# Performance work log

Measured on AMD Instinct MI355X. Metric: run time of the kernel, lower is better.

## Reference

```python
import jax, jax.numpy as jnp
import numpy as np

B, C, H, W = 8, 64, 64, 64
HID = 256  # hidden width of gate_strength_fc


def _init_params(key):
    ks = jax.random.split(key, 12)
    s = 0.05
    p = {}
    p['Wq'] = jax.random.normal(ks[0], (C, C), jnp.float32) * s
    p['bq'] = jnp.zeros((C,), jnp.float32)
    p['Wk'] = jax.random.normal(ks[1], (C, C), jnp.float32) * s
    p['bk'] = jnp.zeros((C,), jnp.float32)
    p['Wv'] = jax.random.normal(ks[2], (C, C), jnp.float32) * s
    p['bv'] = jnp.zeros((C,), jnp.float32)
    p['Wg'] = jax.random.normal(ks[3], (C, C), jnp.float32) * s
    p['bg'] = jnp.zeros((C,), jnp.float32)
    p['W1'] = jax.random.normal(ks[4], (HID, C), jnp.float32) * s
    p['b1'] = jnp.zeros((HID,), jnp.float32)
    p['W2'] = jax.random.normal(ks[5], (1, HID), jnp.float32) * s
    p['b2'] = jnp.zeros((1,), jnp.float32)
    return p


def setup_inputs() -> dict:
    key = jax.random.key(0)
    k0, k1, k2, kp = jax.random.split(key, 4)
    x = jax.random.normal(k0, (B, C, H, W), jnp.float32)
    # torch.rand(...) > 0.8 dropout-style mask, precomputed as 0/1 float for determinism
    mask = (jax.random.uniform(k1, (B, 1, H, W), jnp.float32) > 0.8).astype(jnp.float32)
    use_entropy_gate = jax.random.bernoulli(k2, 0.5, (B,))
    inp = {'x': x, 'mask': mask, 'use_entropy_gate': use_entropy_gate}
    inp.update(_init_params(kp))
    return inp


def _conv1x1(w, b, t):
    # 1x1 conv == per-pixel matmul over channels
    return jnp.einsum('oc,bchw->bohw', w, t) + b[None, :, None, None]


def reference(x, mask, use_entropy_gate, Wq, bq, Wk, bk, Wv, bv, Wg, bg, W1, b1, W2, b2):
    b_, c_, h_, w_ = x.shape
    n = h_ * w_
    masked_x = x * mask
    q = _conv1x1(Wq, bq, masked_x).reshape(b_, c_, n).transpose(0, 2, 1)  # [B,N,C]
    k = _conv1x1(Wk, bk, masked_x).reshape(b_, c_, n)                      # [B,C,N]
    v = _conv1x1(Wv, bv, x).reshape(b_, c_, n)                             # [B,C,N]
    attn = jax.nn.softmax(jnp.einsum('bnc,bcm->bnm', q, k), axis=-1)       # [B,N,N]
    out = jnp.einsum('bcn,bmn->bcm', v, attn).reshape(b_, c_, h_, w_)
    hidden = jax.nn.relu(_conv1x1(W1, b1, x))
    gate_strength = jax.nn.sigmoid(_conv1x1(W2, b2, hidden))               # [B,1,H,W]
    gate = jax.nn.sigmoid(_conv1x1(Wg, bg, x))                             # [B,C,H,W]
    flag = use_entropy_gate[:, None, None, None]
    return jnp.where(flag, out * gate * gate_strength, x)
```

## Files before the change

### kernel.cpp

```cpp
#include <hip/hip_runtime.h>
#include <hip/hip_bf16.h>
#include <math.h>

namespace {
constexpr int kB = 8;
constexpr int kC = 64;
constexpr int kN = 4096;
constexpr int kCap = 1280;
constexpr int kQS = 1312;
constexpr int kSplit = 2;
constexpr long kSeg = (long)kB * kC * kN;
typedef __attribute__((ext_vector_type(8))) short short8;
typedef __attribute__((ext_vector_type(4))) float f32x4;
}

__global__ __launch_bounds__(256) void dense_kernel(
    const float* __restrict__ x, const float* __restrict__ mask,
    const int* __restrict__ flag,
    const float* __restrict__ Wq, const float* __restrict__ bq,
    const float* __restrict__ Wk, const float* __restrict__ bk,
    const float* __restrict__ Wv, const float* __restrict__ bv,
    const float* __restrict__ Wg, const float* __restrict__ bg,
    const float* __restrict__ W1, const float* __restrict__ b1,
    const float* __restrict__ W2, const float* __restrict__ b2,
    __hip_bfloat16* __restrict__ G, float* __restrict__ GS,
    __hip_bfloat16* __restrict__ Qa, __hip_bfloat16* __restrict__ Ka,
    __hip_bfloat16* __restrict__ VaT, float* __restrict__ Sq,
    float* __restrict__ xmsP, int* __restrict__ p2i, int* __restrict__ cnt) {
  const int b = blockIdx.y;
  if (!flag[b]) return;
  const int tile = blockIdx.x;
  const int n0 = tile * 64;
  const int t = threadIdx.x;
  const int wid = t >> 6;
  const int lane = t & 63;

  __shared__ __hip_bfloat16 sWf[4096 * 8];
  __shared__ __hip_bfloat16 sX[64][72];
  __shared__ float sB[512];
  __shared__ float sW2[256];
  __shared__ int sRed[4];
  __shared__ int sI[64];

  {
    const int c = t >> 2;
    const int nn = (t & 3) * 16;
    const float* xp = x + (long)b * kC * kN + (long)c * kN + n0 + nn;
#pragma unroll
    for (int u = 0; u < 16; ++u) sX[nn + u][c] = __float2bfloat16(xp[u]);
  }
  if (t < 64) { sB[t] = bq[t]; sB[64 + t] = bk[t]; sB[128 + t] = bv[t]; sB[192 + t] = bg[t]; }
  sB[256 + t] = b1[t];
  sW2[t] = W2[t];
  for (int f = t; f < 4096; f += 256) {
    const int mt = f >> 7;
    const int ks = (f >> 6) & 1;
    const int ln = f & 63;
    const int m = mt * 16 + (ln & 15);
    const int k0 = ks * 32 + (ln >> 4) * 8;
    const float* Wsrc;
    int row;
    if (m < 64)       { Wsrc = Wq; row = m; }
    else if (m < 128) { Wsrc = Wk; row = m - 64; }
    else if (m < 192) { Wsrc = Wv; row = m - 128; }
    else if (m < 256) { Wsrc = Wg; row = m - 192; }
    else              { Wsrc = W1; row = m - 256; }
#pragma unroll
    for (int j = 0; j < 8; ++j)
      sWf[f * 8 + j] = __float2bfloat16(Wsrc[row * kC + k0 + j]);
  }
  int loc = 0;
  for (int n = t; n < n0; n += 256) loc += (mask[b * kN + n] != 0.f) ? 1 : 0;
#pragma unroll
  for (int d = 1; d < 64; d <<= 1) loc += __shfl_xor(loc, d);
  if (lane == 0) sRed[wid] = loc;
  __syncthreads();
  const int pbase = sRed[0] + sRed[1] + sRed[2] + sRed[3];
  if (wid == 0) {
    const bool a = mask[b * kN + n0 + lane] != 0.f;
    const unsigned long long bal = __ballot(a);
    int ia = a ? (pbase + (int)__popcll(bal & ((1ULL << lane) - 1ULL))) : -1;
    if (ia >= kCap) ia = -1;
    sI[lane] = ia;
    p2i[b * kN + n0 + lane] = ia;
    if (tile == 63 && lane == 0) cnt[b] = pbase + (int)__popcll(bal);
  }
  __syncthreads();

  const int col = lane & 15;
  const int quad = lane >> 4;
  const int nl = wid * 16 + col;
  const int n = n0 + nl;
  const short8 bfr0 = *(const short8*)&sX[nl][quad * 8];
  const short8 bfr1 = *(const short8*)&sX[nl][32 + quad * 8];
  const int i_act = sI[nl];
  const float b2v = b2[0];

  float gs_acc = 0.f;
  float sq_acc = 0.f;
  for (int mt = 0; mt < 32; ++mt) {
    const short8 a0 = *(const short8*)&sWf[((mt * 2 + 0) * 64 + lane) * 8];
    const short8 a1 = *(const short8*)&sWf[((mt * 2 + 1) * 64 + lane) * 8];
    f32x4 acc = {0.f, 0.f, 0.f, 0.f};
    acc = __builtin_amdgcn_mfma_f32_16x16x32_bf16(a0, bfr0, acc, 0, 0, 0);
    acc = __builtin_amdgcn_mfma_f32_16x16x32_bf16(a1, bfr1, acc, 0, 0, 0);
    const int rbase = mt * 16 + quad * 4;
    if (mt < 4) {
      if (i_act >= 0) {
#pragma unroll
        for (int g = 0; g < 4; ++g) {
          const int r = rbase + g;
          const float qv = acc[g] + sB[r];
          Qa[((long)b * kCap + i_act) * kC + r] = __float2bfloat16(qv);
          sq_acc += qv * sB[64 + r];
        }
      }
    } else if (mt < 8) {
      if (i_act >= 0) {
#pragma unroll
        for (int g = 0; g < 4; ++g) {
          const int r = rbase + g;
          Ka[((long)b * kCap + i_act) * kC + (r - 64)] = __float2bfloat16(acc[g] + sB[r]);
        }
      }
    } else if (mt < 12) {
      if (i_act >= 0) {
#pragma unroll
        for (int g = 0; g < 4; ++g) {
          const int r = rbase + g;
          VaT[((long)b * kC + (r - 128)) * kCap + i_act] =
              __float2bfloat16(acc[g] + sB[r]);
        }
      }
    } else if (mt < 16) {
#pragma unroll
      for (int g = 0; g < 4; ++g) {
        const int r = rbase + g;
        const float gv = 1.f / (1.f + __expf(-(acc[g] + sB[r])));
        G[((long)b * kC + (r - 192)) * kN + n] = __float2bfloat16(gv);
      }
    } else {
#pragma unroll
      for (int g = 0; g < 4; ++g) {
        const int r = rbase + g;
        gs_acc += sW2[r - 256] * fmaxf(acc[g] + sB[r], 0.f);
      }
    }
  }
  gs_acc += __shfl_xor(gs_acc, 16);
  gs_acc += __shfl_xor(gs_acc, 32);
  sq_acc += __shfl_xor(sq_acc, 16);
  sq_acc += __shfl_xor(sq_acc, 32);
  if (quad == 0) {
    GS[(long)b * kN + n] = 1.f / (1.f + __expf(-(gs_acc + b2v)));
    if (i_act >= 0) Sq[(long)b * kCap + i_act] = sq_acc;
  }
  {
    const int c = t >> 2;
    const int g4 = t & 3;
    const float* mp = mask + (long)b * kN + n0 + g4 * 16;
    float s = 0.f;
#pragma unroll
    for (int u = 0; u < 16; ++u)
      if (mp[u] == 0.f) s += __bfloat162float(sX[g4 * 16 + u][c]);
    s += __shfl_xor(s, 1);
    s += __shfl_xor(s, 2);
    if (g4 == 0) xmsP[((long)b * 64 + tile) * kC + c] = s;
  }
}

__global__ __launch_bounds__(64) void attn_act_kernel(
    const __hip_bfloat16* __restrict__ Qa, const __hip_bfloat16* __restrict__ Ka,
    const __hip_bfloat16* __restrict__ VaT,
    const int* __restrict__ cnt, const int* __restrict__ flag,
    const float* __restrict__ bq, const float* __restrict__ bk,
    const float* __restrict__ bv, const float* __restrict__ Wv,
    const float* __restrict__ xmsP,
    float* __restrict__ Pm, float* __restrict__ Pl,
    __hip_bfloat16* __restrict__ Po,
    float* __restrict__ Vsum, float* __restrict__ s0M) {
  const int b = blockIdx.z;
  if (!flag[b]) return;
  const int lane = threadIdx.x;

  __shared__ __hip_bfloat16 sP[16][40];
  __shared__ float sxm[kC];

  if (blockIdx.x == kQS / 16) {
    if (blockIdx.y != 0) return;
    float acc = 0.f;
    for (int k = 0; k < 64; ++k) acc += xmsP[((long)b * 64 + k) * kC + lane];
    sxm[lane] = acc;
    __syncthreads();
    float v = 0.f;
#pragma unroll
    for (int o = 0; o < kC; ++o) v += Wv[lane * kC + o] * sxm[o];
    Vsum[b * kC + lane] = v + (float)(kN - cnt[b]) * bv[lane];
    float pp = bq[lane] * bk[lane];
#pragma unroll
    for (int d = 1; d < 64; d <<= 1) pp += __shfl_xor(pp, d);
    if (lane == 0) s0M[0] = pp;
    return;
  }

  const int cc = min(cnt[b], kCap);
  const int ccq = cc + 1;
  const int q0 = blockIdx.x * 16;
  if (q0 >= ccq) return;
  const int s = blockIdx.y;
  const int col = lane & 15;
  const int quad = lane >> 4;
  const int gq = q0 + col;

  const int nT = (cc + 31) >> 5;
  const int tq = (nT + kSplit - 1) / kSplit;
  const int t0 = s * tq;
  const int t1 = min(t0 + tq, nT);
  const long pb = ((long)b * kSplit + s) * kQS + gq;

  if (t0 >= t1) {
    if (gq < ccq) {
      if (quad == 0) { Pm[pb] = -3e38f; Pl[pb] = 0.f; }
#pragma unroll
      for (int ct = 0; ct < 4; ++ct)
#pragma unroll
        for (int g = 0; g < 4; ++g)
          Po[pb * kC + ct * 16 + quad * 4 + g] = __float2bfloat16(0.f);
    }
    return;
  }

  short8 qf0, qf1;
  if (gq == cc) {
#pragma unroll
    for (int j = 0; j < 8; ++j) {
      ((__hip_bfloat16*)&qf0)[j] = __float2bfloat16(bq[quad * 8 + j]);
      ((__hip_bfloat16*)&qf1)[j] = __float2bfloat16(bq[32 + quad * 8 + j]);
    }
  } else {
    const int qrow = (gq < cc) ? gq : (cc - 1);
    const __hip_bfloat16* qr = Qa + ((long)b * kCap + qrow) * kC + quad * 8;
    qf0 = *(const short8*)(qr);
    qf1 = *(const short8*)(qr + 32);
  }

  float Mi = -3e38f, Li = 0.f;
  f32x4 oacc[4];
#pragma unroll
  for (int ct = 0; ct < 4; ++ct) oacc[ct] = (f32x4){0.f, 0.f, 0.f, 0.f};

  for (int kt = t0; kt < t1; ++kt) {
    const int i0 = kt * 32;
    const int kr0 = min(i0 + col, cc - 1);
    const int kr1 = min(i0 + 16 + col, cc - 1);
    const __hip_bfloat16* kp0 = Ka + ((long)b * kCap + kr0) * kC + quad * 8;
    const __hip_bfloat16* kp1 = Ka + ((long)b * kCap + kr1) * kC + quad * 8;
    const short8 kf00 = *(const short8*)(kp0);
    const short8 kf01 = *(const short8*)(kp0 + 32);
    const short8 kf10 = *(const short8*)(kp1);
    const short8 kf11 = *(const short8*)(kp1 + 32);

    f32x4 sa0 = {0.f, 0.f, 0.f, 0.f}, sa1 = {0.f, 0.f, 0.f, 0.f};
    sa0 = __builtin_amdgcn_mfma_f32_16x16x32_bf16(kf00, qf0, sa0, 0, 0, 0);
    sa0 = __builtin_amdgcn_mfma_f32_16x16x32_bf16(kf01, qf1, sa0, 0, 0, 0);
    sa1 = __builtin_amdgcn_mfma_f32_16x16x32_bf16(kf10, qf0, sa1, 0, 0, 0);
    sa1 = __builtin_amdgcn_mfma_f32_16x16x32_bf16(kf11, qf1, sa1, 0, 0, 0);

    float sc[8];
#pragma unroll
    for (int g = 0; g < 4; ++g) {
      sc[g]     = (i0 + quad * 4 + g < cc)      ? sa0[g] : -3e38f;
      sc[4 + g] = (i0 + 16 + quad * 4 + g < cc) ? sa1[g] : -3e38f;
    }
    float lm = sc[0];
#pragma unroll
    for (int u = 1; u < 8; ++u) lm = fmaxf(lm, sc[u]);
    lm = fmaxf(lm, __shfl_xor(lm, 16));
    lm = fmaxf(lm, __shfl_xor(lm, 32));
    const float newM = fmaxf(Mi, lm);
    const float alpha = __expf(Mi - newM);
    float p[8], ps = 0.f;
#pragma unroll
    for (int u = 0; u < 8; ++u) { p[u] = __expf(sc[u] - newM); ps += p[u]; }
    ps += __shfl_xor(ps, 16);
    ps += __shfl_xor(ps, 32);
    Li = Li * alpha + ps;
    Mi = newM;

#pragma unroll
    for (int g = 0; g < 4; ++g) {
      sP[col][quad * 4 + g] = __float2bfloat16(p[g]);
      sP[col][16 + quad * 4 + g] = __float2bfloat16(p[4 + g]);
    }
    __syncthreads();
    const short8 pf = *(const short8*)&sP[col][quad * 8];

#pragma unroll
    for (int ct = 0; ct < 4; ++ct)
#pragma unroll
      for (int g = 0; g < 4; ++g) oacc[ct][g] *= alpha;
#pragma unroll
    for (int ct = 0; ct < 4; ++ct) {
      const short8 vf = *(const short8*)(
          VaT + ((long)b * kC + ct * 16 + col) * kCap + i0 + quad * 8);
      oacc[ct] = __builtin_amdgcn_mfma_f32_16x16x32_bf16(vf, pf, oacc[ct], 0, 0, 0);
    }
    __syncthreads();
  }

  if (gq < ccq) {
    if (quad == 0) { Pm[pb] = Mi; Pl[pb] = Li; }
#pragma unroll
    for (int ct = 0; ct < 4; ++ct)
#pragma unroll
      for (int g = 0; g < 4; ++g)
        Po[pb * kC + ct * 16 + quad * 4 + g] = __float2bfloat16(oacc[ct][g]);
  }
}

__global__ __launch_bounds__(256) void epilogue_kernel(
    const float* __restrict__ x, const int* __restrict__ flag,
    const int* __restrict__ p2i, const int* __restrict__ cnt,
    const float* __restrict__ Pm, const float* __restrict__ Pl,
    const __hip_bfloat16* __restrict__ Po, const float* __restrict__ Sq,
    const float* __restrict__ s0M, const float* __restrict__ Vsum,
    const __hip_bfloat16* __restrict__ G, const float* __restrict__ GS,
    float* __restrict__ out) {
  const int b = blockIdx.z;
  const int cg = blockIdx.y;
  const int n = blockIdx.x * 256 + threadIdx.x;
  const int t = threadIdx.x;
  const long bbase = (long)b * kC * kN + n;
  if (!flag[b]) {
#pragma unroll
    for (int u = 0; u < 16; ++u) {
      const long a = bbase + (long)(cg * 16 + u) * kN;
      out[a] = x[a];
    }
    return;
  }
  const int cTrue = cnt[b];
  const int cc = min(cTrue, kCap);
  const float multF = (float)(kN - cTrue);

  __shared__ float sFac[kSplit + 1];
  __shared__ float sOM16[16];
  __shared__ float sVs[16];
  if (t == 0) {
    const float s0 = s0M[0];
    float mar[kSplit], lar[kSplit];
    float M = s0;
#pragma unroll
    for (int s = 0; s < kSplit; ++s) {
      const long pbs = ((long)b * kSplit + s) * kQS + cc;
      mar[s] = Pm[pbs];
      lar[s] = Pl[pbs];
      M = fmaxf(M, mar[s]);
    }
    const float p0 = __expf(s0 - M);
    float L = multF * p0;
    float wgt[kSplit];
#pragma unroll
    for (int s = 0; s < kSplit; ++s) { wgt[s] = __expf(mar[s] - M); L += lar[s] * wgt[s]; }
    const float invL = 1.f / L;
#pragma unroll
    for (int s = 0; s < kSplit; ++s) sFac[s] = wgt[s] * invL;
    sFac[kSplit] = p0 * invL;
  }
  if (t < 16) sVs[t] = Vsum[b * kC + cg * 16 + t];
  __syncthreads();
  if (t < 16) {
    const int c = cg * 16 + t;
    float o = sFac[kSplit] * sVs[t];
#pragma unroll
    for (int s = 0; s < kSplit; ++s)
      o += sFac[s] * __bfloat162float(Po[(((long)b * kSplit + s) * kQS + cc) * kC + c]);
    sOM16[t] = o;
  }
  __syncthreads();

  const float gsv = GS[(long)b * kN + n];
  const int i = p2i[b * kN + n];
  float r16[16];
  if (i >= 0) {
    const float s0 = Sq[(long)b * kCap + i];
    float mar[kSplit], lar[kSplit];
    float M = s0;
#pragma unroll
    for (int s = 0; s < kSplit; ++s) {
      const long pbs = ((long)b * kSplit + s) * kQS + i;
      mar[s] = Pm[pbs];
      lar[s] = Pl[pbs];
      M = fmaxf(M, mar[s]);
    }
    const float p0 = __expf(s0 - M);
    float L = multF * p0;
    float fac[kSplit];
#pragma unroll
    for (int s = 0; s < kSplit; ++s) { fac[s] = __expf(mar[s] - M); L += lar[s] * fac[s]; }
    const float invL = 1.f / L;
    const float facP = p0 * invL;
#pragma unroll
    for (int u = 0; u < 16; ++u) r16[u] = facP * sVs[u];
#pragma unroll
    for (int s = 0; s < kSplit; ++s) {
      const float f = fac[s] * invL;
      const __hip_bfloat16* pr =
          Po + (((long)b * kSplit + s) * kQS + i) * kC + cg * 16;
      const short8 po0 = *(const short8*)(pr);
      const short8 po1 = *(const short8*)(pr + 8);
#pragma unroll
      for (int u = 0; u < 8; ++u) {
        r16[u]     += f * __bfloat162float(((const __hip_bfloat16*)&po0)[u]);
        r16[8 + u] += f * __bfloat162float(((const __hip_bfloat16*)&po1)[u]);
      }
    }
  } else {
#pragma unroll
    for (int u = 0; u < 16; ++u) r16[u] = sOM16[u];
  }
#pragma unroll
  for (int u = 0; u < 16; ++u) {
    const long a = bbase + (long)(cg * 16 + u) * kN;
    out[a] = r16[u] * __bfloat162float(G[a]) * gsv;
  }
}

extern "C" void kernel_launch(void* const* d_in, const int* in_sizes, int n_in,
                              void* d_out, int out_size, void* d_ws, size_t ws_size,
                              hipStream_t stream) {
  (void)in_sizes; (void)n_in; (void)out_size; (void)ws_size;
  const float* x    = (const float*)d_in[0];
  const float* mask = (const float*)d_in[1];
  const int*   flag = (const int*)d_in[2];
  const float* Wq = (const float*)d_in[3];
  const float* bq = (const float*)d_in[4];
  const float* Wk = (const float*)d_in[5];
  const float* bk = (const float*)d_in[6];
  const float* Wv = (const float*)d_in[7];
  const float* bv = (const float*)d_in[8];
  const float* Wg = (const float*)d_in[9];
  const float* bg = (const float*)d_in[10];
  const float* W1 = (const float*)d_in[11];
  const float* b1 = (const float*)d_in[12];
  const float* W2 = (const float*)d_in[13];
  const float* b2 = (const float*)d_in[14];
  float* out = (float*)d_out;

  char* w = (char*)d_ws;
  float* GS = (float*)w;                       w += (long)kB * kN * 4;
  __hip_bfloat16* G  = (__hip_bfloat16*)w;     w += kSeg * 2;
  __hip_bfloat16* Qa = (__hip_bfloat16*)w;     w += (long)kB * kCap * kC * 2;
  __hip_bfloat16* Ka = (__hip_bfloat16*)w;     w += (long)kB * kCap * kC * 2;
  __hip_bfloat16* VaT= (__hip_bfloat16*)w;     w += (long)kB * kC * kCap * 2;
  __hip_bfloat16* Po = (__hip_bfloat16*)w;     w += (long)kB * kSplit * kQS * kC * 2;
  float* Pm = (float*)w;                       w += (long)kB * kSplit * kQS * 4;
  float* Pl = (float*)w;                       w += (long)kB * kSplit * kQS * 4;
  float* Sq = (float*)w;                       w += (long)kB * kCap * 4;
  float* xmsP = (float*)w;                     w += (long)kB * 64 * kC * 4;
  int* p2i = (int*)w;                          w += (long)kB * kN * 4;
  int* cnt = (int*)w;                          w += 64;
  float* Vsum = (float*)w;                     w += kB * kC * 4;
  float* s0M  = (float*)w;                     w += 64;

  dim3 gd(64, kB);
  dense_kernel<<<gd, 256, 0, stream>>>(x, mask, flag, Wq, bq, Wk, bk, Wv, bv,
                                       Wg, bg, W1, b1, W2, b2,
                                       G, GS, Qa, Ka, VaT, Sq, xmsP, p2i, cnt);
  dim3 gat(kQS / 16 + 1, kSplit, kB);
  attn_act_kernel<<<gat, 64, 0, stream>>>(Qa, Ka, VaT, cnt, flag, bq, bk, bv, Wv,
                                          xmsP, Pm, Pl, Po, Vsum, s0M);
  dim3 gep(kN / 256, 4, kB);
  epilogue_kernel<<<gep, 256, 0, stream>>>(x, flag, p2i, cnt, Pm, Pl, Po, Sq,
                                           s0M, Vsum, G, GS, out);
}
```

Baseline: 122.4 us.

## Split attention key tiles across 8 waves per block with in-LDS merge

Replaces the 2-way split-K across separate 64-thread blocks with 512-thread blocks whose 8 waves each process interleaved key tiles. The waves merge their online-softmax partials (max, sum, output) through shared memory, so the epilogue reads one partial instead of combining several. K fragments for the next tile are prefetched and V loads are issued early. The __syncthreads in the loop become a wave-local LDS wait. The aim is more parallelism per query tile and less partial-result traffic. In exchange, each block uses more LDS and pays a cross-wave reduction step.

```diff
diff --git a/kernel.cpp b/kernel.cpp
--- a/kernel.cpp
+++ b/kernel.cpp
@@ -8,7 +8,7 @@
 constexpr int kN = 4096;
 constexpr int kCap = 1280;
 constexpr int kQS = 1312;
-constexpr int kSplit = 2;
+constexpr int kW = 8;
 constexpr long kSeg = (long)kB * kC * kN;
 typedef __attribute__((ext_vector_type(8))) short short8;
 typedef __attribute__((ext_vector_type(4))) float f32x4;
@@ -169,7 +169,7 @@
   }
 }
 
-__global__ __launch_bounds__(64) void attn_act_kernel(
+__global__ __launch_bounds__(512) void attn_act_kernel(
     const __hip_bfloat16* __restrict__ Qa, const __hip_bfloat16* __restrict__ Ka,
     const __hip_bfloat16* __restrict__ VaT,
     const int* __restrict__ cnt, const int* __restrict__ flag,
@@ -179,22 +179,19 @@
     float* __restrict__ Pm, float* __restrict__ Pl,
     __hip_bfloat16* __restrict__ Po,
     float* __restrict__ Vsum, float* __restrict__ s0M) {
-  const int b = blockIdx.z;
+  const int b = blockIdx.y;
   if (!flag[b]) return;
-  const int lane = threadIdx.x;
-
-  __shared__ __hip_bfloat16 sP[16][40];
-  __shared__ float sxm[kC];
+  const int t = threadIdx.x;
+  const int wid = t >> 6;
+  const int lane = t & 63;
 
   if (blockIdx.x == kQS / 16) {
-    if (blockIdx.y != 0) return;
+    if (wid != 0) return;
     float acc = 0.f;
     for (int k = 0; k < 64; ++k) acc += xmsP[((long)b * 64 + k) * kC + lane];
-    sxm[lane] = acc;
-    __syncthreads();
     float v = 0.f;
 #pragma unroll
-    for (int o = 0; o < kC; ++o) v += Wv[lane * kC + o] * sxm[o];
+    for (int o = 0; o < kC; ++o) v += Wv[lane * kC + o] * __shfl(acc, o);
     Vsum[b * kC + lane] = v + (float)(kN - cnt[b]) * bv[lane];
     float pp = bq[lane] * bk[lane];
 #pragma unroll
@@ -207,28 +204,15 @@
   const int ccq = cc + 1;
   const int q0 = blockIdx.x * 16;
   if (q0 >= ccq) return;
-  const int s = blockIdx.y;
+
+  __shared__ __hip_bfloat16 sP[kW][16][40];
+  __shared__ float sM[kW][16];
+  __shared__ float sL[kW][16];
+  __shared__ float sO[kW][16][68];
+
   const int col = lane & 15;
   const int quad = lane >> 4;
   const int gq = q0 + col;
-
-  const int nT = (cc + 31) >> 5;
-  const int tq = (nT + kSplit - 1) / kSplit;
-  const int t0 = s * tq;
-  const int t1 = min(t0 + tq, nT);
-  const long pb = ((long)b * kSplit + s) * kQS + gq;
-
-  if (t0 >= t1) {
-    if (gq < ccq) {
-      if (quad == 0) { Pm[pb] = -3e38f; Pl[pb] = 0.f; }
-#pragma unroll
-      for (int ct = 0; ct < 4; ++ct)
-#pragma unroll
-        for (int g = 0; g < 4; ++g)
-          Po[pb * kC + ct * 16 + quad * 4 + g] = __float2bfloat16(0.f);
-    }
-    return;
-  }
 
   short8 qf0, qf1;
   if (gq == cc) {
@@ -244,21 +228,45 @@
     qf1 = *(const short8*)(qr + 32);
   }
 
+  const int nT = (cc + 31) >> 5;
   float Mi = -3e38f, Li = 0.f;
   f32x4 oacc[4];
 #pragma unroll
   for (int ct = 0; ct < 4; ++ct) oacc[ct] = (f32x4){0.f, 0.f, 0.f, 0.f};
 
-  for (int kt = t0; kt < t1; ++kt) {
+  int kt = wid;
+  short8 kf00, kf01, kf10, kf11;
+  if (kt < nT) {
     const int i0 = kt * 32;
     const int kr0 = min(i0 + col, cc - 1);
     const int kr1 = min(i0 + 16 + col, cc - 1);
     const __hip_bfloat16* kp0 = Ka + ((long)b * kCap + kr0) * kC + quad * 8;
     const __hip_bfloat16* kp1 = Ka + ((long)b * kCap + kr1) * kC + quad * 8;
-    const short8 kf00 = *(const short8*)(kp0);
-    const short8 kf01 = *(const short8*)(kp0 + 32);
-    const short8 kf10 = *(const short8*)(kp1);
-    const short8 kf11 = *(const short8*)(kp1 + 32);
+    kf00 = *(const short8*)(kp0);
+    kf01 = *(const short8*)(kp0 + 32);
+    kf10 = *(const short8*)(kp1);
+    kf11 = *(const short8*)(kp1 + 32);
+  }
+
+  while (kt < nT) {
+    const int i0 = kt * 32;
+    short8 vf0 = *(const short8*)(VaT + ((long)b * kC + 0  + col) * kCap + i0 + quad * 8);
+    short8 vf1 = *(const short8*)(VaT + ((long)b * kC + 16 + col) * kCap + i0 + quad * 8);
+    short8 vf2 = *(const short8*)(VaT + ((long)b * kC + 32 + col) * kCap + i0 + quad * 8);
+    short8 vf3 = *(const short8*)(VaT + ((long)b * kC + 48 + col) * kCap + i0 + quad * 8);
+    const int ktn = kt + kW;
+    short8 nk00, nk01, nk10, nk11;
+    if (ktn < nT) {
+      const int j0 = ktn * 32;
+      const int kr0 = min(j0 + col, cc - 1);
+      const int kr1 = min(j0 + 16 + col, cc - 1);
+      const __hip_bfloat16* kp0 = Ka + ((long)b * kCap + kr0) * kC + quad * 8;
+      const __hip_bfloat16* kp1 = Ka + ((long)b * kCap + kr1) * kC + quad * 8;
+      nk00 = *(const short8*)(kp0);
+      nk01 = *(const short8*)(kp0 + 32);
+      nk10 = *(const short8*)(kp1);
+      nk11 = *(const short8*)(kp1 + 32);
+    }
 
     f32x4 sa0 = {0.f, 0.f, 0.f, 0.f}, sa1 = {0.f, 0.f, 0.f, 0.f};
     sa0 = __builtin_amdgcn_mfma_f32_16x16x32_bf16(kf00, qf0, sa0, 0, 0, 0);
@@ -289,32 +297,50 @@
 
 #pragma unroll
     for (int g = 0; g < 4; ++g) {
-      sP[col][quad * 4 + g] = __float2bfloat16(p[g]);
-      sP[col][16 + quad * 4 + g] = __float2bfloat16(p[4 + g]);
-    }
-    __syncthreads();
-    const short8 pf = *(const short8*)&sP[col][quad * 8];
+      sP[wid][col][quad * 4 + g] = __float2bfloat16(p[g]);
+      sP[wid][col][16 + quad * 4 + g] = __float2bfloat16(p[4 + g]);
+    }
+    asm volatile("s_waitcnt lgkmcnt(0)" ::: "memory");
+    __builtin_amdgcn_sched_barrier(0);
+    const short8 pf = *(const short8*)&sP[wid][col][quad * 8];
 
 #pragma unroll
     for (int ct = 0; ct < 4; ++ct)
 #pragma unroll
       for (int g = 0; g < 4; ++g) oacc[ct][g] *= alpha;
-#pragma unroll
-    for (int ct = 0; ct < 4; ++ct) {
-      const short8 vf = *(const short8*)(
-          VaT + ((long)b * kC + ct * 16 + col) * kCap + i0 + quad * 8);
-      oacc[ct] = __builtin_amdgcn_mfma_f32_16x16x32_bf16(vf, pf, oacc[ct], 0, 0, 0);
-    }
-    __syncthreads();
-  }
-
-  if (gq < ccq) {
-    if (quad == 0) { Pm[pb] = Mi; Pl[pb] = Li; }
-#pragma unroll
-    for (int ct = 0; ct < 4; ++ct)
-#pragma unroll
-      for (int g = 0; g < 4; ++g)
-        Po[pb * kC + ct * 16 + quad * 4 + g] = __float2bfloat16(oacc[ct][g]);
+    oacc[0] = __builtin_amdgcn_mfma_f32_16x16x32_bf16(vf0, pf, oacc[0], 0, 0, 0);
+    oacc[1] = __builtin_amdgcn_mfma_f32_16x16x32_bf16(vf1, pf, oacc[1], 0, 0, 0);
+    oacc[2] = __builtin_amdgcn_mfma_f32_16x16x32_bf16(vf2, pf, oacc[2], 0, 0, 0);
+    oacc[3] = __builtin_amdgcn_mfma_f32_16x16x32_bf16(vf3, pf, oacc[3], 0, 0, 0);
+
+    kf00 = nk00; kf01 = nk01; kf10 = nk10; kf11 = nk11;
+    kt = ktn;
+  }
+
+  if (quad == 0) { sM[wid][col] = Mi; sL[wid][col] = Li; }
+#pragma unroll
+  for (int ct = 0; ct < 4; ++ct)
+    *(f32x4*)&sO[wid][col][ct * 16 + quad * 4] = oacc[ct];
+  __syncthreads();
+
+  {
+    const int mq = t >> 5;
+    const int c0 = (t & 31) * 2;
+    float Mt = sM[0][mq];
+#pragma unroll
+    for (int w = 1; w < kW; ++w) Mt = fmaxf(Mt, sM[w][mq]);
+    float Lt = 0.f, o0 = 0.f, o1 = 0.f;
+#pragma unroll
+    for (int w = 0; w < kW; ++w) {
+      const float g = __expf(sM[w][mq] - Mt);
+      Lt += g * sL[w][mq];
+      o0 += g * sO[w][mq][c0];
+      o1 += g * sO[w][mq][c0 + 1];
+    }
+    const long pb = (long)b * kQS + (q0 + mq);
+    if (c0 == 0) { Pm[pb] = Mt; Pl[pb] = Lt; }
+    Po[pb * kC + c0]     = __float2bfloat16(o0);
+    Po[pb * kC + c0 + 1] = __float2bfloat16(o1);
   }
 }
 
@@ -343,39 +369,21 @@
   const int cc = min(cTrue, kCap);
   const float multF = (float)(kN - cTrue);
 
-  __shared__ float sFac[kSplit + 1];
   __shared__ float sOM16[16];
   __shared__ float sVs[16];
-  if (t == 0) {
-    const float s0 = s0M[0];
-    float mar[kSplit], lar[kSplit];
-    float M = s0;
-#pragma unroll
-    for (int s = 0; s < kSplit; ++s) {
-      const long pbs = ((long)b * kSplit + s) * kQS + cc;
-      mar[s] = Pm[pbs];
-      lar[s] = Pl[pbs];
-      M = fmaxf(M, mar[s]);
-    }
-    const float p0 = __expf(s0 - M);
-    float L = multF * p0;
-    float wgt[kSplit];
-#pragma unroll
-    for (int s = 0; s < kSplit; ++s) { wgt[s] = __expf(mar[s] - M); L += lar[s] * wgt[s]; }
-    const float invL = 1.f / L;
-#pragma unroll
-    for (int s = 0; s < kSplit; ++s) sFac[s] = wgt[s] * invL;
-    sFac[kSplit] = p0 * invL;
-  }
-  if (t < 16) sVs[t] = Vsum[b * kC + cg * 16 + t];
-  __syncthreads();
   if (t < 16) {
     const int c = cg * 16 + t;
-    float o = sFac[kSplit] * sVs[t];
-#pragma unroll
-    for (int s = 0; s < kSplit; ++s)
-      o += sFac[s] * __bfloat162float(Po[(((long)b * kSplit + s) * kQS + cc) * kC + c]);
-    sOM16[t] = o;
+    const float vs = Vsum[b * kC + c];
+    sVs[t] = vs;
+    const float s0 = s0M[0];
+    const long pb = (long)b * kQS + cc;
+    const float M1 = Pm[pb], L1 = Pl[pb];
+    const float Mt = fmaxf(M1, s0);
+    const float w1 = __expf(M1 - Mt);
+    const float p0 = __expf(s0 - Mt);
+    const float invL = 1.f / (w1 * L1 + multF * p0);
+    sOM16[t] = p0 * invL * vs +
+               w1 * invL * __bfloat162float(Po[pb * kC + c]);
   }
   __syncthreads();
 
@@ -384,36 +392,21 @@
   float r16[16];
   if (i >= 0) {
     const float s0 = Sq[(long)b * kCap + i];
-    float mar[kSplit], lar[kSplit];
-    float M = s0;
-#pragma unroll
-    for (int s = 0; s < kSplit; ++s) {
-      const long pbs = ((long)b * kSplit + s) * kQS + i;
-      mar[s] = Pm[pbs];
-      lar[s] = Pl[pbs];
-      M = fmaxf(M, mar[s]);
-    }
-    const float p0 = __expf(s0 - M);
-    float L = multF * p0;
-    float fac[kSplit];
-#pragma unroll
-    for (int s = 0; s < kSplit; ++s) { fac[s] = __expf(mar[s] - M); L += lar[s] * fac[s]; }
-    const float invL = 1.f / L;
-    const float facP = p0 * invL;
-#pragma unroll
-    for (int u = 0; u < 16; ++u) r16[u] = facP * sVs[u];
-#pragma unroll
-    for (int s = 0; s < kSplit; ++s) {
-      const float f = fac[s] * invL;
-      const __hip_bfloat16* pr =
-          Po + (((long)b * kSplit + s) * kQS + i) * kC + cg * 16;
-      const short8 po0 = *(const short8*)(pr);
-      const short8 po1 = *(const short8*)(pr + 8);
-#pragma unroll
-      for (int u = 0; u < 8; ++u) {
-        r16[u]     += f * __bfloat162float(((const __hip_bfloat16*)&po0)[u]);
-        r16[8 + u] += f * __bfloat162float(((const __hip_bfloat16*)&po1)[u]);
-      }
+    const long pb = (long)b * kQS + i;
+    const float M1 = Pm[pb], L1 = Pl[pb];
+    const float Mt = fmaxf(M1, s0);
+    const float w1 = __expf(M1 - Mt);
+    const float p0 = __expf(s0 - Mt);
+    const float invL = 1.f / (w1 * L1 + multF * p0);
+    const float f1 = w1 * invL;
+    const float fP = p0 * invL;
+    const __hip_bfloat16* pr = Po + pb * kC + cg * 16;
+    const short8 po0 = *(const short8*)(pr);
+    const short8 po1 = *(const short8*)(pr + 8);
+#pragma unroll
+    for (int u = 0; u < 8; ++u) {
+      r16[u]     = fP * sVs[u]     + f1 * __bfloat162float(((const __hip_bfloat16*)&po0)[u]);
+      r16[8 + u] = fP * sVs[8 + u] + f1 * __bfloat162float(((const __hip_bfloat16*)&po1)[u]);
     }
   } else {
 #pragma unroll
@@ -453,9 +446,9 @@
   __hip_bfloat16* Qa = (__hip_bfloat16*)w;     w += (long)kB * kCap * kC * 2;
   __hip_bfloat16* Ka = (__hip_bfloat16*)w;     w += (long)kB * kCap * kC * 2;
   __hip_bfloat16* VaT= (__hip_bfloat16*)w;     w += (long)kB * kC * kCap * 2;
-  __hip_bfloat16* Po = (__hip_bfloat16*)w;     w += (long)kB * kSplit * kQS * kC * 2;
-  float* Pm = (float*)w;                       w += (long)kB * kSplit * kQS * 4;
-  float* Pl = (float*)w;                       w += (long)kB * kSplit * kQS * 4;
+  __hip_bfloat16* Po = (__hip_bfloat16*)w;     w += (long)kB * kQS * kC * 2;
+  float* Pm = (float*)w;                       w += (long)kB * kQS * 4;
+  float* Pl = (float*)w;                       w += (long)kB * kQS * 4;
   float* Sq = (float*)w;                       w += (long)kB * kCap * 4;
   float* xmsP = (float*)w;                     w += (long)kB * 64 * kC * 4;
   int* p2i = (int*)w;                          w += (long)kB * kN * 4;
@@ -467,9 +460,9 @@
   dense_kernel<<<gd, 256, 0, stream>>>(x, mask, flag, Wq, bq, Wk, bk, Wv, bv,
                                        Wg, bg, W1, b1, W2, b2,
                                        G, GS, Qa, Ka, VaT, Sq, xmsP, p2i, cnt);
-  dim3 gat(kQS / 16 + 1, kSplit, kB);
-  attn_act_kernel<<<gat, 64, 0, stream>>>(Qa, Ka, VaT, cnt, flag, bq, bk, bv, Wv,
-                                          xmsP, Pm, Pl, Po, Vsum, s0M);
+  dim3 gat(kQS / 16 + 1, kB);
+  attn_act_kernel<<<gat, 512, 0, stream>>>(Qa, Ka, VaT, cnt, flag, bq, bk, bv, Wv,
+                                           xmsP, Pm, Pl, Po, Vsum, s0M);
   dim3 gep(kN / 256, 4, kB);
   epilogue_kernel<<<gep, 256, 0, stream>>>(x, flag, p2i, cnt, Pm, Pl, Po, Sq,
                                            s0M, Vsum, G, GS, out);
```

Result: slower. 125.1 us (+2.2%).
